# Kernel tuning notes

Hardware: AMD Instinct MI355X
Metric: run time of the kernel (lower is better)

## Reference

```python
import jax, jax.numpy as jnp
import numpy as np

EMBED = 1024
HEADS = 16
HEAD_DIM = EMBED // HEADS
FF = 4 * EMBED
B, S = 2, 2048
EPS = 1e-5


def layer_norm(x, g, b):
    mu = jnp.mean(x, axis=-1, keepdims=True)
    var = jnp.mean(jnp.square(x - mu), axis=-1, keepdims=True)
    return (x - mu) * jax.lax.rsqrt(var + EPS) * g + b


def setup_inputs() -> dict:
    key = jax.random.key(0)
    ks = jax.random.split(key, 12)
    sc = 0.02
    x = jax.random.normal(ks[0], (B, S, EMBED), dtype=jnp.float32)
    # causal mask: 1 where attending allowed (mask==0 -> -inf in original)
    mask = jnp.tril(jnp.ones((S, S), dtype=jnp.int32))[None, None]
    return {
        "x": x,
        "mask": mask,
        "ln1_g": jnp.ones((EMBED,), jnp.float32),
        "ln1_b": jnp.zeros((EMBED,), jnp.float32),
        "wq": sc * jax.random.normal(ks[1], (EMBED, EMBED), jnp.float32),
        "bq": jnp.zeros((EMBED,), jnp.float32),
        "wk": sc * jax.random.normal(ks[2], (EMBED, EMBED), jnp.float32),
        "bk": jnp.zeros((EMBED,), jnp.float32),
        "wv": sc * jax.random.normal(ks[3], (EMBED, EMBED), jnp.float32),
        "bv": jnp.zeros((EMBED,), jnp.float32),
        "wo": sc * jax.random.normal(ks[4], (EMBED, EMBED), jnp.float32),
        "bo": jnp.zeros((EMBED,), jnp.float32),
        "ln2_g": jnp.ones((EMBED,), jnp.float32),
        "ln2_b": jnp.zeros((EMBED,), jnp.float32),
        "w1": sc * jax.random.normal(ks[5], (EMBED, FF), jnp.float32),
        "b1": jnp.zeros((FF,), jnp.float32),
        "w2": sc * jax.random.normal(ks[6], (FF, EMBED), jnp.float32),
        "b2": jnp.zeros((EMBED,), jnp.float32),
    }


def reference(x, mask, ln1_g, ln1_b, wq, bq, wk, bk, wv, bv, wo, bo,
              ln2_g, ln2_b, w1, b1, w2, b2):
    bsz, seq, _ = x.shape
    residual = x
    h = layer_norm(x, ln1_g, ln1_b)
    # QKV projections -> [B, H, S, Dh]
    def split_heads(t):
        return t.reshape(bsz, seq, HEADS, HEAD_DIM).transpose(0, 2, 1, 3)
    q = split_heads(h @ wq + bq)
    k = split_heads(h @ wk + bk)
    v = split_heads(h @ wv + bv)
    scores = jnp.einsum('bhqd,bhkd->bhqk', q, k) / (HEAD_DIM ** 0.5)
    scores = jnp.where(mask == 0, -jnp.inf, scores)
    attn = jax.nn.softmax(scores, axis=-1)
    out = jnp.einsum('bhqk,bhkd->bhqd', attn, v)
    out = out.transpose(0, 2, 1, 3).reshape(bsz, seq, EMBED)
    out = out @ wo + bo
    x = residual + out
    residual = x
    h = layer_norm(x, ln2_g, ln2_b)
    h = jax.nn.gelu(h @ w1 + b1, approximate=False) @ w2 + b2
    return residual + h
```

## Files before the change

### kernel.cpp

```cpp
#include <hip/hip_runtime.h>

typedef unsigned short u16;
typedef unsigned int   u32;
typedef __attribute__((ext_vector_type(8))) short bf16x8;
typedef __attribute__((ext_vector_type(4))) float f32x4;

#define S_LEN 2048
#define EMB   1024
#define NH    16
#define HD    64
#define FF_DIM 4096
#define NROWS 4096

__device__ __forceinline__ float b2f(u16 u){ union{u32 i; float f;} c; c.i = ((u32)u)<<16; return c.f; }
__device__ __forceinline__ u16 f2b(float f){ union{float f; u32 u;} c; c.f=f; return (u16)((c.u + 0x8000u)>>16); }
__device__ __forceinline__ float gelu_f(float x){
    float z  = x * 0.70710678118f;
    float az = fabsf(z);
    float t  = 1.0f / (1.0f + 0.3275911f * az);
    float p  = ((((1.061405429f*t - 1.453152027f)*t + 1.421413741f)*t - 0.284496736f)*t + 0.254829592f)*t;
    float e  = __expf(-az*az);
    float erfv = 1.0f - p*e;
    erfv = (z < 0.f) ? -erfv : erfv;
    return 0.5f*x*(1.0f + erfv);
}

__device__ __forceinline__ void load_lds16(const u16* g, u16* l) {
    __builtin_amdgcn_global_load_lds((const __attribute__((address_space(1))) u32*)g,
                                     (__attribute__((address_space(3))) u32*)l, 16, 0, 0);
}

template<int XF32>
__global__ __launch_bounds__(256)
void ln_kernel(const void* __restrict__ Xv, const float* __restrict__ G,
               const float* __restrict__ Bv, u16* __restrict__ Y)
{
    const int row = blockIdx.x, t = threadIdx.x;
    float v0, v1, v2, v3;
    if constexpr (XF32) {
        float4 r4 = ((const float4*)((const float*)Xv + (size_t)row*EMB))[t];
        v0 = r4.x; v1 = r4.y; v2 = r4.z; v3 = r4.w;
    } else {
        const u16* xr = (const u16*)Xv + (size_t)row*EMB;
        uint2 raw = *(const uint2*)(xr + t*4);
        v0 = b2f(raw.x & 0xffff); v1 = b2f(raw.x >> 16);
        v2 = b2f(raw.y & 0xffff); v3 = b2f(raw.y >> 16);
    }
    float s  = v0+v1+v2+v3;
    float s2 = v0*v0+v1*v1+v2*v2+v3*v3;
    #pragma unroll
    for (int off = 1; off < 64; off <<= 1) {
        s  += __shfl_xor(s,  off, 64);
        s2 += __shfl_xor(s2, off, 64);
    }
    __shared__ float ps[4], ps2[4];
    const int w = t >> 6, lane = t & 63;
    if (lane == 0) { ps[w] = s; ps2[w] = s2; }
    __syncthreads();
    s  = ps[0]+ps[1]+ps[2]+ps[3];
    s2 = ps2[0]+ps2[1]+ps2[2]+ps2[3];
    const float mu   = s * (1.0f/EMB);
    const float rstd = rsqrtf(fmaxf(s2*(1.0f/EMB) - mu*mu, 0.f) + 1e-5f);
    float4 g4 = ((const float4*)G)[t];
    float4 c4 = ((const float4*)Bv)[t];
    u32 lo = (u32)f2b((v0-mu)*rstd*g4.x + c4.x) | ((u32)f2b((v1-mu)*rstd*g4.y + c4.y) << 16);
    u32 hi = (u32)f2b((v2-mu)*rstd*g4.z + c4.z) | ((u32)f2b((v3-mu)*rstd*g4.w + c4.w) << 16);
    uint2 o; o.x = lo; o.y = hi;
    *(uint2*)(Y + (size_t)row*EMB + t*4) = o;
}

__global__ __launch_bounds__(256)
void transpose_k(const float* __restrict__ in, u16* __restrict__ out, int K, int N)
{
    __shared__ __align__(16) u16 T[64*72];
    const int k0 = blockIdx.y*64, n0 = blockIdx.x*64, t = threadIdx.x;
    #pragma unroll
    for (int c = 0; c < 4; ++c) {
        int e = t*4 + c*1024, ki = e >> 6, nj = e & 63;
        float4 f = *(const float4*)(in + (size_t)(k0+ki)*N + n0 + nj);
        ushort4 s4; s4.x = f2b(f.x); s4.y = f2b(f.y); s4.z = f2b(f.z); s4.w = f2b(f.w);
        *(ushort4*)&T[ki*72 + nj] = s4;
    }
    __syncthreads();
    #pragma unroll
    for (int c = 0; c < 2; ++c) {
        int e = t*8 + c*2048, ni = e >> 6, kj = e & 63;
        uint4 v; u16* pv = (u16*)&v;
        #pragma unroll
        for (int j = 0; j < 8; ++j) pv[j] = T[(kj+j)*72 + ni];
        *(uint4*)(out + (size_t)(n0+ni)*K + k0 + kj) = v;
    }
}

__global__ __launch_bounds__(256)
void vtrans(const u16* __restrict__ in, u16* __restrict__ out)
{
    __shared__ __align__(16) u16 T[64*72];
    const int bh = blockIdx.y, s0 = blockIdx.x*64, t = threadIdx.x;
    const size_t base = (size_t)bh * (S_LEN*HD);
    #pragma unroll
    for (int c = 0; c < 2; ++c) {
        int e = t*8 + c*2048, r = e >> 6, d = e & 63;
        *(uint4*)&T[r*72 + d] = *(const uint4*)(in + base + (size_t)(s0 + r)*HD + d);
    }
    __syncthreads();
    #pragma unroll
    for (int c = 0; c < 2; ++c) {
        int e = t*8 + c*2048, d = e >> 6, sj = e & 63;
        uint4 v; u16* pv = (u16*)&v;
        #pragma unroll
        for (int j = 0; j < 8; ++j) pv[j] = T[(sj + j)*72 + d];
        *(uint4*)(out + base + (size_t)d*S_LEN + s0 + sj) = v;
    }
}

__device__ __forceinline__ void stage2(const u16* s0, const u16* s1, int koff, u16* dst, int wave){
    load_lds16(s0 + koff, dst + wave*512);
    load_lds16(s1 + koff, dst + 4096 + wave*512);
}

template<int CBUF, int KS, int NHH, int TAILVM>
__device__ __forceinline__ void phase256(u16* Ls, f32x4 (&acc)[8][4],
    int wm, int wn, int lr, int quad, int wave,
    const u16* s0, const u16* s1, int koff, u16* dst)
{
    const u16* ak = Ls + CBUF*32768 + KS*8192;
    const u16* bk = Ls + CBUF*32768 + 16384 + KS*8192;
    bf16x8 af[8], bf[2];
    #pragma unroll
    for (int mf = 0; mf < 8; ++mf) {
        int off = (wm*128 + mf*16 + lr)*32 + quad*8;
        af[mf] = *(const bf16x8*)(ak + (off ^ ((off>>3)&0x18)));
    }
    #pragma unroll
    for (int nf = 0; nf < 2; ++nf) {
        int off = (wn*64 + NHH*32 + nf*16 + lr)*32 + quad*8;
        bf[nf] = *(const bf16x8*)(bk + (off ^ ((off>>3)&0x18)));
    }
    stage2(s0, s1, koff, dst, wave);
    __builtin_amdgcn_s_barrier();
    __builtin_amdgcn_s_setprio(1);
    #pragma unroll
    for (int mf = 0; mf < 8; ++mf) {
        acc[mf][NHH*2+0] = __builtin_amdgcn_mfma_f32_16x16x32_bf16(af[mf], bf[0], acc[mf][NHH*2+0], 0, 0, 0);
        acc[mf][NHH*2+1] = __builtin_amdgcn_mfma_f32_16x16x32_bf16(af[mf], bf[1], acc[mf][NHH*2+1], 0, 0, 0);
    }
    __builtin_amdgcn_s_setprio(0);
    if constexpr (TAILVM) asm volatile("s_waitcnt vmcnt(8)" ::: "memory");
    __builtin_amdgcn_s_barrier();
}

template<int MODE>
__global__ __launch_bounds__(512, 2)
void gemm256(const u16* __restrict__ A, const u16* __restrict__ Bt,
             const float* __restrict__ bias, const float* __restrict__ bias2,
             const float* __restrict__ bias3,
             void* __restrict__ C, void* __restrict__ C2, void* __restrict__ C3,
             int M, int N, int K)
{
    (void)M;
    __shared__ __align__(16) u16 Ls[65536];
    const int t = threadIdx.x;
    const int wave = t >> 6, lane = t & 63;
    const int wm = wave >> 2, wn = wave & 3;
    const int lr = lane & 15, quad = lane >> 4;
    const int n0 = blockIdx.x*256, m0 = blockIdx.y*256;

    const int c0 = wave*64 + lane, c1 = 512 + wave*64 + lane;
    const int l0 = c0 ^ ((c0 >> 3) & 3), l1 = c1 ^ ((c1 >> 3) & 3);
    const int r0 = l0 >> 2, g0 = l0 & 3;
    const int r1 = l1 >> 2, g1 = l1 & 3;
    const u16* srcA0 = A  + (size_t)(m0 + r0)*K + g0*8;
    const u16* srcA1 = A  + (size_t)(m0 + r1)*K + g1*8;
    const u16* srcB0 = Bt + (size_t)(n0 + r0)*K + g0*8;
    const u16* srcB1 = Bt + (size_t)(n0 + r1)*K + g1*8;

    u16* A00 = Ls + 0;
    u16* A01 = Ls + 8192;
    u16* B00 = Ls + 16384;
    u16* B01 = Ls + 16384 + 8192;
    u16* A10 = Ls + 32768;
    u16* A11 = Ls + 32768 + 8192;
    u16* B10 = Ls + 32768 + 16384;
    u16* B11 = Ls + 32768 + 16384 + 8192;

    f32x4 acc[8][4];
    const f32x4 fzero = {0.f, 0.f, 0.f, 0.f};
    #pragma unroll
    for (int i = 0; i < 8; ++i)
        #pragma unroll
        for (int j = 0; j < 4; ++j) acc[i][j] = fzero;

    const int NT = K >> 6;

    stage2(srcA0, srcA1, 0,   A00, wave);
    stage2(srcB0, srcB1, 0,   B00, wave);
    stage2(srcA0, srcA1, 32,  A01, wave);
    stage2(srcB0, srcB1, 32,  B01, wave);
    stage2(srcA0, srcA1, 64,  A10, wave);
    stage2(srcB0, srcB1, 64,  B10, wave);
    asm volatile("s_waitcnt vmcnt(8)" ::: "memory");
    __builtin_amdgcn_s_barrier();

    for (int U = 0; U < NT; U += 2) {
        const int k1 = ((U+1) & (NT-1))*64;
        const int k2 = ((U+2) & (NT-1))*64;
        const int k3 = ((U+3) & (NT-1))*64;
        phase256<0,0,0,0>(Ls, acc, wm, wn, lr, quad, wave, srcA0, srcA1, k1+32, A11);
        phase256<0,0,1,1>(Ls, acc, wm, wn, lr, quad, wave, srcB0, srcB1, k1+32, B11);
        phase256<0,1,0,0>(Ls, acc, wm, wn, lr, quad, wave, srcA0, srcA1, k2,    A00);
        phase256<0,1,1,1>(Ls, acc, wm, wn, lr, quad, wave, srcB0, srcB1, k2,    B00);
        phase256<1,0,0,0>(Ls, acc, wm, wn, lr, quad, wave, srcA0, srcA1, k2+32, A01);
        phase256<1,0,1,1>(Ls, acc, wm, wn, lr, quad, wave, srcB0, srcB1, k2+32, B01);
        phase256<1,1,0,0>(Ls, acc, wm, wn, lr, quad, wave, srcA0, srcA1, k3,    A10);
        phase256<1,1,1,1>(Ls, acc, wm, wn, lr, quad, wave, srcB0, srcB1, k3,    B10);
    }

    asm volatile("s_waitcnt vmcnt(0)" ::: "memory");
    __syncthreads();

    float bv[4];
    #pragma unroll
    for (int nf = 0; nf < 4; ++nf) {
        const int col = n0 + wn*64 + nf*16 + lr;
        if constexpr (MODE == 5) {
            const int seg = n0 >> 10;
            bv[nf] = (seg == 0 ? bias : (seg == 1 ? bias2 : bias3))[col & 1023];
        } else {
            bv[nf] = bias[col];
        }
    }
    #pragma unroll
    for (int mf = 0; mf < 8; ++mf)
        #pragma unroll
        for (int nf = 0; nf < 4; ++nf)
            #pragma unroll
            for (int r = 0; r < 4; ++r) {
                float v = acc[mf][nf][r] + bv[nf];
                if constexpr (MODE == 2) v = gelu_f(v);
                Ls[(wm*128 + mf*16 + quad*4 + r)*256 + wn*64 + nf*16 + lr] = f2b(v);
            }
    __syncthreads();
    #pragma unroll
    for (int j = 0; j < 16; ++j) {
        const int idx = j*512 + t;
        const int rr = idx >> 5, ck = idx & 31;
        const u16* src = Ls + rr*256 + ck*8;
        const int row = m0 + rr, col = n0 + ck*8;
        if constexpr (MODE == 5) {
            const int seg = n0 >> 10;
            u16* dstb = (u16*)(seg == 0 ? C : (seg == 1 ? C2 : C3));
            const int cs = col & 1023;
            const int h = cs >> 6, d = cs & 63;
            const int b_ = row >> 11, s = row & 2047;
            *(uint4*)(dstb + ((((size_t)(b_*NH + h))*S_LEN + s) << 6) + d) = *(const uint4*)src;
        } else {
            *(uint4*)((u16*)C + (size_t)row*N + col) = *(const uint4*)src;
        }
    }
}

template<int MODE, int RESF, int OUTF, int TM>
__global__ __launch_bounds__(256)
void gemm_bt(const u16* __restrict__ A, const u16* __restrict__ Bt,
             const float* __restrict__ bias, const float* __restrict__ bias2,
             const float* __restrict__ bias3, const void* __restrict__ res,
             void* __restrict__ C, void* __restrict__ C2, void* __restrict__ C3,
             int M, int N, int K)
{
    constexpr int MT  = (TM == 128) ? 4 : 2;
    constexpr int ACH = TM * 32;
    __shared__ __align__(16) u16 Sm[(TM == 128) ? 16384 : 12288];
    u16* As = Sm;
    u16* Bs = Sm + 2*ACH;
    const int t = threadIdx.x;
    const int m0 = (TM == 128) ? blockIdx.y*128 : blockIdx.x*64;
    const int n0 = (TM == 128) ? blockIdx.x*128 : blockIdx.y*128;
    const int wave = t >> 6, lane = t & 63;
    const int wm = (wave >> 1) * (TM/2);
    const int wn = (wave & 1) * 64;
    const int lr = lane & 15, quad = lane >> 4;

    const u16* gA = A  + (size_t)(m0 + wave*16 + (lane >> 2))*K + (lane & 3)*8;
    const u16* gB = Bt + (size_t)(n0 + wave*16 + (lane >> 2))*K + (lane & 3)*8;
    u16* lA = As + wave*512;
    u16* lB = Bs + wave*512;

    f32x4 acc[MT][4];
    const f32x4 fzero = {0.f, 0.f, 0.f, 0.f};
    #pragma unroll
    for (int mt = 0; mt < MT; ++mt)
        #pragma unroll
        for (int nt = 0; nt < 4; ++nt) acc[mt][nt] = fzero;

    for (int kt = 0; kt < K; kt += 64) {
        __syncthreads();
        #pragma unroll
        for (int c = 0; c < 2; ++c) {
            load_lds16(gA + c*32, lA + c*ACH);
            if constexpr (TM == 128)
                load_lds16(gA + (size_t)64*K + c*32, lA + c*ACH + 2048);
            load_lds16(gB + c*32, lB + c*4096);
            load_lds16(gB + (size_t)64*K + c*32, lB + c*4096 + 2048);
        }
        gA += 64; gB += 64;
        __syncthreads();
        #pragma unroll
        for (int ks = 0; ks < 2; ++ks) {
            bf16x8 af[MT], bf[4];
            #pragma unroll
            for (int i = 0; i < MT; ++i)
                af[i] = *(const bf16x8*)&As[ks*ACH + (wm + i*16 + lr)*32 + quad*8];
            #pragma unroll
            for (int i = 0; i < 4; ++i)
                bf[i] = *(const bf16x8*)&Bs[ks*4096 + (wn + i*16 + lr)*32 + quad*8];
            #pragma unroll
            for (int mt = 0; mt < MT; ++mt)
                #pragma unroll
                for (int nt = 0; nt < 4; ++nt)
                    acc[mt][nt] = __builtin_amdgcn_mfma_f32_16x16x32_bf16(af[mt], bf[nt], acc[mt][nt], 0, 0, 0);
        }
    }

    u16* qkvDst = nullptr;
    if constexpr (MODE == 5) {
        int seg = n0 >> 10;
        qkvDst = (u16*)(seg == 0 ? C : (seg == 1 ? C2 : C3));
    }

    #pragma unroll
    for (int c = 0; c < (TM == 128 ? 2 : 1); ++c) {
        __syncthreads();
        if (TM == 64 || (wave >> 1) == c) {
            #pragma unroll
            for (int nt = 0; nt < 4; ++nt) {
                int colL = wn + nt*16 + lr;
                float bval;
                if constexpr (MODE == 5) {
                    int col = n0 + colL;
                    int seg = col >> 10, cs = col & 1023;
                    bval = (seg == 0 ? bias : (seg == 1 ? bias2 : bias3))[cs];
                } else {
                    bval = bias[n0 + colL];
                }
                #pragma unroll
                for (int mt = 0; mt < MT; ++mt) {
                    #pragma unroll
                    for (int r = 0; r < 4; ++r) {
                        int rowL = (TM == 128 ? mt*16 : wm + mt*16) + quad*4 + r;
                        float v = acc[mt][nt][r] + bval;
                        if constexpr (MODE == 2) v = gelu_f(v);
                        Sm[rowL*136 + colL] = f2b(v);
                    }
                }
            }
        }
        __syncthreads();
        #pragma unroll
        for (int i = 0; i < 4; ++i) {
            const int rowL = wave*16 + i*4 + (lane >> 4);
            const int colL = (lane & 15)*8;
            const int row  = m0 + c*64 + rowL;
            const u16* src = &Sm[rowL*136 + colL];
            if constexpr (MODE == 5) {
                int cs = (n0 + colL) & 1023;
                int h = cs >> 6, d = cs & 63;
                int b_ = row >> 11, s = row & 2047;
                u16* dst = qkvDst + ((((size_t)(b_*NH + h))*S_LEN + s) << 6) + d;
                *(uint4*)dst = *(const uint4*)src;
            } else {
                size_t base = (size_t)row*N + n0 + colL;
                if constexpr (MODE == 1 || OUTF) {
                    uint4 sv = *(const uint4*)src;
                    const u16* sp = (const u16*)&sv;
                    float f[8];
                    #pragma unroll
                    for (int j = 0; j < 8; ++j) f[j] = b2f(sp[j]);
                    if constexpr (MODE == 1) {
                        if constexpr (RESF) {
                            const float* rp = (const float*)res + base;
                            float4 r0 = *(const float4*)rp, r1 = *(const float4*)(rp+4);
                            f[0]+=r0.x; f[1]+=r0.y; f[2]+=r0.z; f[3]+=r0.w;
                            f[4]+=r1.x; f[5]+=r1.y; f[6]+=r1.z; f[7]+=r1.w;
                        } else {
                            uint4 rv = *(const uint4*)((const u16*)res + base);
                            const u16* rp = (const u16*)&rv;
                            #pragma unroll
                            for (int j = 0; j < 8; ++j) f[j] += b2f(rp[j]);
                        }
                    }
                    if constexpr (OUTF) {
                        float* op = (float*)C + base;
                        float4 o0 = {f[0],f[1],f[2],f[3]}, o1 = {f[4],f[5],f[6],f[7]};
                        *(float4*)op = o0; *(float4*)(op+4) = o1;
                    } else {
                        u16 ov[8];
                        #pragma unroll
                        for (int j = 0; j < 8; ++j) ov[j] = f2b(f[j]);
                        *(uint4*)((u16*)C + base) = *(const uint4*)ov;
                    }
                } else {
                    *(uint4*)((u16*)C + base) = *(const uint4*)src;
                }
            }
        }
    }
}

__global__ __launch_bounds__(256, 2)
void attn_kernel(const u16* __restrict__ Q, const u16* __restrict__ Kg,
                 const u16* __restrict__ Vt, u16* __restrict__ O)
{
    const int bh = blockIdx.x;
    const int pr = blockIdx.y;
    const int qta = pr, qtb = 31 - pr;
    const int t = threadIdx.x, wave = t >> 6, lane = t & 63;
    const int lr = lane & 15, quad = lane >> 4;

    __shared__ __align__(16) u16 Ks[4096];
    __shared__ __align__(16) u16 Vs[4096];
    __shared__ __align__(16) u16 Ps[4][16*72];

    const size_t qkbase = (size_t)bh * (S_LEN*HD);
    const int b = bh >> 4, h = bh & 15;
    u16* Pw = Ps[wave];
    const f32x4 fzero = {0.f, 0.f, 0.f, 0.f};

    const u16* qpa = Q + qkbase + (size_t)(qta*64 + wave*16 + lr)*HD + quad*8;
    const u16* qpb = Q + qkbase + (size_t)(qtb*64 + wave*16 + lr)*HD + quad*8;
    bf16x8 qa0 = *(const bf16x8*)qpa, qa1 = *(const bf16x8*)(qpa + 32);
    bf16x8 qb0 = *(const bf16x8*)qpb, qb1 = *(const bf16x8*)(qpb + 32);

    f32x4 oa[4], ob[4];
    float la[4], lb[4];
    #pragma unroll
    for (int dt = 0; dt < 4; ++dt) { oa[dt] = fzero; ob[dt] = fzero; }
    #pragma unroll
    for (int r = 0; r < 4; ++r) { la[r] = 0.f; lb[r] = 0.f; }

    const u16* gK = Kg + qkbase + (size_t)(wave*16 + (lane>>2))*HD + (lane&3)*8;
    const u16* gV = Vt + qkbase + (size_t)(wave*16 + (lane>>2))*S_LEN + (lane&3)*8;
    u16* lK = Ks + wave*512;
    u16* lV = Vs + wave*512;

    const int qrow_qa = qta*64 + wave*16 + quad*4;
    const int qrow_qb = qtb*64 + wave*16 + quad*4;

    for (int kb = 0; kb <= qtb; ++kb) {
        __syncthreads();
        load_lds16(gK + (size_t)kb*4096,      lK);
        load_lds16(gK + (size_t)kb*4096 + 32, lK + 2048);
        load_lds16(gV + kb*64,                lV);
        load_lds16(gV + kb*64 + 32,           lV + 2048);
        __syncthreads();

        #pragma unroll
        for (int tile = 0; tile < 2; ++tile) {
            const int qt = tile ? qta : qtb;
            if (tile && kb > qta) break;
            bf16x8 qf0 = tile ? qa0 : qb0;
            bf16x8 qf1 = tile ? qa1 : qb1;
            f32x4* oacc = tile ? oa : ob;
            float* lp   = tile ? la : lb;
            const int qrowq = tile ? qrow_qa : qrow_qb;

            f32x4 sc[4];
            #pragma unroll
            for (int kt2 = 0; kt2 < 4; ++kt2) {
                bf16x8 kf0 = *(const bf16x8*)&Ks[(kt2*16 + lr)*32 + quad*8];
                bf16x8 kf1 = *(const bf16x8*)&Ks[2048 + (kt2*16 + lr)*32 + quad*8];
                sc[kt2] = __builtin_amdgcn_mfma_f32_16x16x32_bf16(qf0, kf0, fzero, 0, 0, 0);
                sc[kt2] = __builtin_amdgcn_mfma_f32_16x16x32_bf16(qf1, kf1, sc[kt2], 0, 0, 0);
            }
            const bool diag = (kb == qt);
            #pragma unroll
            for (int r = 0; r < 4; ++r) {
                #pragma unroll
                for (int kt2 = 0; kt2 < 4; ++kt2) {
                    int kcol = kb*64 + kt2*16 + lr;
                    float p = (!diag || kcol <= qrowq + r) ? __expf(fminf(sc[kt2][r]*0.125f, 30.f)) : 0.f;
                    lp[r] += p;
                    Pw[(quad*4 + r)*72 + kt2*16 + lr] = f2b(p);
                }
            }
            bf16x8 pf0 = *(const bf16x8*)&Pw[lr*72 + quad*8];
            bf16x8 pf1 = *(const bf16x8*)&Pw[lr*72 + 32 + quad*8];
            #pragma unroll
            for (int dt = 0; dt < 4; ++dt) {
                bf16x8 vf0 = *(const bf16x8*)&Vs[(dt*16 + lr)*32 + quad*8];
                bf16x8 vf1 = *(const bf16x8*)&Vs[2048 + (dt*16 + lr)*32 + quad*8];
                oacc[dt] = __builtin_amdgcn_mfma_f32_16x16x32_bf16(pf0, vf0, oacc[dt], 0, 0, 0);
                oacc[dt] = __builtin_amdgcn_mfma_f32_16x16x32_bf16(pf1, vf1, oacc[dt], 0, 0, 0);
            }
        }
    }

    #pragma unroll
    for (int tile = 0; tile < 2; ++tile) {
        const int qt = tile ? qta : qtb;
        f32x4* oacc = tile ? oa : ob;
        float* lp   = tile ? la : lb;
        #pragma unroll
        for (int r = 0; r < 4; ++r) {
            float v = lp[r];
            v += __shfl_xor(v, 1, 64); v += __shfl_xor(v, 2, 64);
            v += __shfl_xor(v, 4, 64); v += __shfl_xor(v, 8, 64);
            lp[r] = 1.0f / fmaxf(v, 1e-20f);
        }
        #pragma unroll
        for (int dt = 0; dt < 4; ++dt)
            #pragma unroll
            for (int r = 0; r < 4; ++r)
                Pw[(quad*4 + r)*64 + dt*16 + lr] = f2b(oacc[dt][r] * lp[r]);

        const int q = lane >> 2, d0 = (lane & 3)*16;
        u16* dst = O + ((size_t)(b*S_LEN + qt*64 + wave*16 + q))*EMB + h*HD + d0;
        *(uint4*)(dst)     = *(uint4*)&Pw[q*64 + d0];
        *(uint4*)(dst + 8) = *(uint4*)&Pw[q*64 + d0 + 8];
    }
}

extern "C" void kernel_launch(void* const* d_in, const int* in_sizes, int n_in,
                              void* d_out, int out_size, void* d_ws, size_t ws_size,
                              hipStream_t stream)
{
    (void)in_sizes; (void)n_in; (void)out_size; (void)ws_size;
    const float* x    = (const float*)d_in[0];
    const float* ln1g = (const float*)d_in[2];
    const float* ln1b = (const float*)d_in[3];
    const float* wq = (const float*)d_in[4];  const float* bq = (const float*)d_in[5];
    const float* wk = (const float*)d_in[6];  const float* bk = (const float*)d_in[7];
    const float* wv = (const float*)d_in[8];  const float* bv = (const float*)d_in[9];
    const float* wo = (const float*)d_in[10]; const float* bo = (const float*)d_in[11];
    const float* ln2g = (const float*)d_in[12]; const float* ln2b = (const float*)d_in[13];
    const float* w1 = (const float*)d_in[14]; const float* b1 = (const float*)d_in[15];
    const float* w2 = (const float*)d_in[16]; const float* b2 = (const float*)d_in[17];

    u16* ws = (u16*)d_ws;
    const size_t M1 = 1u << 20;
    u16* wqkvT = ws + 0*M1;
    u16* wqT = ws + 0*M1;
    u16* wkT = ws + 1*M1;
    u16* wvT = ws + 2*M1;
    u16* woT = ws + 3*M1;
    u16* w2T = ws + 0*M1;
    u16* w1T = ws + 4*M1;
    u16* h0  = ws + 8*M1;
    u16* qb  = ws + 12*M1;
    u16* kb  = ws + 16*M1;
    u16* vT  = ws + 20*M1;
    u16* ao  = ws + 24*M1;
    u16* vb  = ws + 24*M1;
    u16* x1  = ws + 28*M1;
    u16* fb  = ws + 12*M1;

    dim3 blk(256);
    transpose_k<<<dim3(16,16), blk, 0, stream>>>(wq, wqT, EMB, EMB);
    transpose_k<<<dim3(16,16), blk, 0, stream>>>(wk, wkT, EMB, EMB);
    transpose_k<<<dim3(16,16), blk, 0, stream>>>(wv, wvT, EMB, EMB);
    transpose_k<<<dim3(16,16), blk, 0, stream>>>(wo, woT, EMB, EMB);
    transpose_k<<<dim3(64,16), blk, 0, stream>>>(w1, w1T, EMB, FF_DIM);

    ln_kernel<1><<<NROWS, blk, 0, stream>>>(x, ln1g, ln1b, h0);

    gemm256<5><<<dim3(12,16), dim3(512), 0, stream>>>(h0, wqkvT, bq, bk, bv,
                                                      qb, kb, vb, NROWS, 3072, EMB);

    vtrans<<<dim3(32,32), blk, 0, stream>>>(vb, vT);

    attn_kernel<<<dim3(32,16), blk, 0, stream>>>(qb, kb, vT, ao);

    gemm_bt<1,1,0,64><<<dim3(64,8), blk, 0, stream>>>(ao, woT, bo, nullptr, nullptr, x,
                                                      x1, nullptr, nullptr, NROWS, EMB, EMB);

    transpose_k<<<dim3(16,64), blk, 0, stream>>>(w2, w2T, FF_DIM, EMB);

    ln_kernel<0><<<NROWS, blk, 0, stream>>>(x1, ln2g, ln2b, h0);

    gemm256<2><<<dim3(16,16), dim3(512), 0, stream>>>(h0, w1T, b1, nullptr, nullptr,
                                                      fb, nullptr, nullptr, NROWS, FF_DIM, EMB);

    gemm_bt<1,0,1,64><<<dim3(64,8), blk, 0, stream>>>(fb, w2T, b2, nullptr, nullptr, x1,
                                                      d_out, nullptr, nullptr, NROWS, EMB, FF_DIM);
}
```

Baseline: 374.6 us.

## Use split-K 256x256 pipelined GEMM with reduction kernels for Wo and FF2

Replaces the simple 64x128-tile GEMM used for the output projection and the second feed-forward layer with the pipelined 256x256-tile GEMM core. K is split four ways to give 256 blocks. Each split writes bf16 partial sums, and separate elementwise kernels add the partials, bias and residual. The main loop is factored into a shared device function. This adds extra global traffic for the partials and extra launches. Storing partials in bf16 reduces accuracy, and the output buffer is reused as scratch space.

```diff
diff --git a/kernel.cpp b/kernel.cpp
--- a/kernel.cpp
+++ b/kernel.cpp
@@ -150,31 +150,10 @@
     __builtin_amdgcn_s_barrier();
 }
 
-template<int MODE>
-__global__ __launch_bounds__(512, 2)
-void gemm256(const u16* __restrict__ A, const u16* __restrict__ Bt,
-             const float* __restrict__ bias, const float* __restrict__ bias2,
-             const float* __restrict__ bias3,
-             void* __restrict__ C, void* __restrict__ C2, void* __restrict__ C3,
-             int M, int N, int K)
-{
-    (void)M;
-    __shared__ __align__(16) u16 Ls[65536];
-    const int t = threadIdx.x;
-    const int wave = t >> 6, lane = t & 63;
-    const int wm = wave >> 2, wn = wave & 3;
-    const int lr = lane & 15, quad = lane >> 4;
-    const int n0 = blockIdx.x*256, m0 = blockIdx.y*256;
-
-    const int c0 = wave*64 + lane, c1 = 512 + wave*64 + lane;
-    const int l0 = c0 ^ ((c0 >> 3) & 3), l1 = c1 ^ ((c1 >> 3) & 3);
-    const int r0 = l0 >> 2, g0 = l0 & 3;
-    const int r1 = l1 >> 2, g1 = l1 & 3;
-    const u16* srcA0 = A  + (size_t)(m0 + r0)*K + g0*8;
-    const u16* srcA1 = A  + (size_t)(m0 + r1)*K + g1*8;
-    const u16* srcB0 = Bt + (size_t)(n0 + r0)*K + g0*8;
-    const u16* srcB1 = Bt + (size_t)(n0 + r1)*K + g1*8;
-
+__device__ __forceinline__ void gemm256_main(u16* Ls, f32x4 (&acc)[8][4],
+    int wm, int wn, int lr, int quad, int wave, int NT,
+    const u16* srcA0, const u16* srcA1, const u16* srcB0, const u16* srcB1)
+{
     u16* A00 = Ls + 0;
     u16* A01 = Ls + 8192;
     u16* B00 = Ls + 16384;
@@ -183,15 +162,6 @@
     u16* A11 = Ls + 32768 + 8192;
     u16* B10 = Ls + 32768 + 16384;
     u16* B11 = Ls + 32768 + 16384 + 8192;
-
-    f32x4 acc[8][4];
-    const f32x4 fzero = {0.f, 0.f, 0.f, 0.f};
-    #pragma unroll
-    for (int i = 0; i < 8; ++i)
-        #pragma unroll
-        for (int j = 0; j < 4; ++j) acc[i][j] = fzero;
-
-    const int NT = K >> 6;
 
     stage2(srcA0, srcA1, 0,   A00, wave);
     stage2(srcB0, srcB1, 0,   B00, wave);
@@ -218,6 +188,41 @@
 
     asm volatile("s_waitcnt vmcnt(0)" ::: "memory");
     __syncthreads();
+}
+
+template<int MODE>
+__global__ __launch_bounds__(512, 2)
+void gemm256(const u16* __restrict__ A, const u16* __restrict__ Bt,
+             const float* __restrict__ bias, const float* __restrict__ bias2,
+             const float* __restrict__ bias3,
+             void* __restrict__ C, void* __restrict__ C2, void* __restrict__ C3,
+             int M, int N, int K)
+{
+    (void)M;
+    __shared__ __align__(16) u16 Ls[65536];
+    const int t = threadIdx.x;
+    const int wave = t >> 6, lane = t & 63;
+    const int wm = wave >> 2, wn = wave & 3;
+    const int lr = lane & 15, quad = lane >> 4;
+    const int n0 = blockIdx.x*256, m0 = blockIdx.y*256;
+
+    const int c0 = wave*64 + lane, c1 = 512 + wave*64 + lane;
+    const int l0 = c0 ^ ((c0 >> 3) & 3), l1 = c1 ^ ((c1 >> 3) & 3);
+    const int r0 = l0 >> 2, g0 = l0 & 3;
+    const int r1 = l1 >> 2, g1 = l1 & 3;
+    const u16* srcA0 = A  + (size_t)(m0 + r0)*K + g0*8;
+    const u16* srcA1 = A  + (size_t)(m0 + r1)*K + g1*8;
+    const u16* srcB0 = Bt + (size_t)(n0 + r0)*K + g0*8;
+    const u16* srcB1 = Bt + (size_t)(n0 + r1)*K + g1*8;
+
+    f32x4 acc[8][4];
+    const f32x4 fzero = {0.f, 0.f, 0.f, 0.f};
+    #pragma unroll
+    for (int i = 0; i < 8; ++i)
+        #pragma unroll
+        for (int j = 0; j < 4; ++j) acc[i][j] = fzero;
+
+    gemm256_main(Ls, acc, wm, wn, lr, quad, wave, K >> 6, srcA0, srcA1, srcB0, srcB1);
 
     float bv[4];
     #pragma unroll
@@ -260,151 +265,113 @@
     }
 }
 
-template<int MODE, int RESF, int OUTF, int TM>
+__global__ __launch_bounds__(512, 2)
+void gemm256sk(const u16* __restrict__ A, const u16* __restrict__ Bt,
+               u16* __restrict__ Cl, u16* __restrict__ Ch, int N, int K)
+{
+    __shared__ __align__(16) u16 Ls[65536];
+    const int t = threadIdx.x;
+    const int wave = t >> 6, lane = t & 63;
+    const int wm = wave >> 2, wn = wave & 3;
+    const int lr = lane & 15, quad = lane >> 4;
+    const int n0 = blockIdx.x*256, m0 = blockIdx.y*256;
+    const int z  = blockIdx.z;
+    const int Ks = K >> 2;
+
+    const int c0 = wave*64 + lane, c1 = 512 + wave*64 + lane;
+    const int l0 = c0 ^ ((c0 >> 3) & 3), l1 = c1 ^ ((c1 >> 3) & 3);
+    const int r0 = l0 >> 2, g0 = l0 & 3;
+    const int r1 = l1 >> 2, g1 = l1 & 3;
+    const u16* srcA0 = A  + (size_t)(m0 + r0)*K + g0*8 + z*Ks;
+    const u16* srcA1 = A  + (size_t)(m0 + r1)*K + g1*8 + z*Ks;
+    const u16* srcB0 = Bt + (size_t)(n0 + r0)*K + g0*8 + z*Ks;
+    const u16* srcB1 = Bt + (size_t)(n0 + r1)*K + g1*8 + z*Ks;
+
+    f32x4 acc[8][4];
+    const f32x4 fzero = {0.f, 0.f, 0.f, 0.f};
+    #pragma unroll
+    for (int i = 0; i < 8; ++i)
+        #pragma unroll
+        for (int j = 0; j < 4; ++j) acc[i][j] = fzero;
+
+    gemm256_main(Ls, acc, wm, wn, lr, quad, wave, Ks >> 6, srcA0, srcA1, srcB0, srcB1);
+
+    #pragma unroll
+    for (int mf = 0; mf < 8; ++mf)
+        #pragma unroll
+        for (int nf = 0; nf < 4; ++nf)
+            #pragma unroll
+            for (int r = 0; r < 4; ++r)
+                Ls[(wm*128 + mf*16 + quad*4 + r)*256 + wn*64 + nf*16 + lr] = f2b(acc[mf][nf][r]);
+    __syncthreads();
+    u16* dst = (z < 2 ? Cl : Ch) + (size_t)(z & 1)*(1u<<22);
+    #pragma unroll
+    for (int j = 0; j < 16; ++j) {
+        const int idx = j*512 + t;
+        const int rr = idx >> 5, ck = idx & 31;
+        *(uint4*)(dst + (size_t)(m0 + rr)*N + n0 + ck*8) = *(const uint4*)(Ls + rr*256 + ck*8);
+    }
+}
+
 __global__ __launch_bounds__(256)
-void gemm_bt(const u16* __restrict__ A, const u16* __restrict__ Bt,
-             const float* __restrict__ bias, const float* __restrict__ bias2,
-             const float* __restrict__ bias3, const void* __restrict__ res,
-             void* __restrict__ C, void* __restrict__ C2, void* __restrict__ C3,
-             int M, int N, int K)
-{
-    constexpr int MT  = (TM == 128) ? 4 : 2;
-    constexpr int ACH = TM * 32;
-    __shared__ __align__(16) u16 Sm[(TM == 128) ? 16384 : 12288];
-    u16* As = Sm;
-    u16* Bs = Sm + 2*ACH;
-    const int t = threadIdx.x;
-    const int m0 = (TM == 128) ? blockIdx.y*128 : blockIdx.x*64;
-    const int n0 = (TM == 128) ? blockIdx.x*128 : blockIdx.y*128;
-    const int wave = t >> 6, lane = t & 63;
-    const int wm = (wave >> 1) * (TM/2);
-    const int wn = (wave & 1) * 64;
-    const int lr = lane & 15, quad = lane >> 4;
-
-    const u16* gA = A  + (size_t)(m0 + wave*16 + (lane >> 2))*K + (lane & 3)*8;
-    const u16* gB = Bt + (size_t)(n0 + wave*16 + (lane >> 2))*K + (lane & 3)*8;
-    u16* lA = As + wave*512;
-    u16* lB = Bs + wave*512;
-
-    f32x4 acc[MT][4];
-    const f32x4 fzero = {0.f, 0.f, 0.f, 0.f};
-    #pragma unroll
-    for (int mt = 0; mt < MT; ++mt)
-        #pragma unroll
-        for (int nt = 0; nt < 4; ++nt) acc[mt][nt] = fzero;
-
-    for (int kt = 0; kt < K; kt += 64) {
-        __syncthreads();
-        #pragma unroll
-        for (int c = 0; c < 2; ++c) {
-            load_lds16(gA + c*32, lA + c*ACH);
-            if constexpr (TM == 128)
-                load_lds16(gA + (size_t)64*K + c*32, lA + c*ACH + 2048);
-            load_lds16(gB + c*32, lB + c*4096);
-            load_lds16(gB + (size_t)64*K + c*32, lB + c*4096 + 2048);
-        }
-        gA += 64; gB += 64;
-        __syncthreads();
-        #pragma unroll
-        for (int ks = 0; ks < 2; ++ks) {
-            bf16x8 af[MT], bf[4];
-            #pragma unroll
-            for (int i = 0; i < MT; ++i)
-                af[i] = *(const bf16x8*)&As[ks*ACH + (wm + i*16 + lr)*32 + quad*8];
-            #pragma unroll
-            for (int i = 0; i < 4; ++i)
-                bf[i] = *(const bf16x8*)&Bs[ks*4096 + (wn + i*16 + lr)*32 + quad*8];
-            #pragma unroll
-            for (int mt = 0; mt < MT; ++mt)
-                #pragma unroll
-                for (int nt = 0; nt < 4; ++nt)
-                    acc[mt][nt] = __builtin_amdgcn_mfma_f32_16x16x32_bf16(af[mt], bf[nt], acc[mt][nt], 0, 0, 0);
-        }
-    }
-
-    u16* qkvDst = nullptr;
-    if constexpr (MODE == 5) {
-        int seg = n0 >> 10;
-        qkvDst = (u16*)(seg == 0 ? C : (seg == 1 ? C2 : C3));
-    }
-
-    #pragma unroll
-    for (int c = 0; c < (TM == 128 ? 2 : 1); ++c) {
-        __syncthreads();
-        if (TM == 64 || (wave >> 1) == c) {
-            #pragma unroll
-            for (int nt = 0; nt < 4; ++nt) {
-                int colL = wn + nt*16 + lr;
-                float bval;
-                if constexpr (MODE == 5) {
-                    int col = n0 + colL;
-                    int seg = col >> 10, cs = col & 1023;
-                    bval = (seg == 0 ? bias : (seg == 1 ? bias2 : bias3))[cs];
-                } else {
-                    bval = bias[n0 + colL];
-                }
-                #pragma unroll
-                for (int mt = 0; mt < MT; ++mt) {
-                    #pragma unroll
-                    for (int r = 0; r < 4; ++r) {
-                        int rowL = (TM == 128 ? mt*16 : wm + mt*16) + quad*4 + r;
-                        float v = acc[mt][nt][r] + bval;
-                        if constexpr (MODE == 2) v = gelu_f(v);
-                        Sm[rowL*136 + colL] = f2b(v);
-                    }
-                }
-            }
-        }
-        __syncthreads();
-        #pragma unroll
-        for (int i = 0; i < 4; ++i) {
-            const int rowL = wave*16 + i*4 + (lane >> 4);
-            const int colL = (lane & 15)*8;
-            const int row  = m0 + c*64 + rowL;
-            const u16* src = &Sm[rowL*136 + colL];
-            if constexpr (MODE == 5) {
-                int cs = (n0 + colL) & 1023;
-                int h = cs >> 6, d = cs & 63;
-                int b_ = row >> 11, s = row & 2047;
-                u16* dst = qkvDst + ((((size_t)(b_*NH + h))*S_LEN + s) << 6) + d;
-                *(uint4*)dst = *(const uint4*)src;
-            } else {
-                size_t base = (size_t)row*N + n0 + colL;
-                if constexpr (MODE == 1 || OUTF) {
-                    uint4 sv = *(const uint4*)src;
-                    const u16* sp = (const u16*)&sv;
-                    float f[8];
-                    #pragma unroll
-                    for (int j = 0; j < 8; ++j) f[j] = b2f(sp[j]);
-                    if constexpr (MODE == 1) {
-                        if constexpr (RESF) {
-                            const float* rp = (const float*)res + base;
-                            float4 r0 = *(const float4*)rp, r1 = *(const float4*)(rp+4);
-                            f[0]+=r0.x; f[1]+=r0.y; f[2]+=r0.z; f[3]+=r0.w;
-                            f[4]+=r1.x; f[5]+=r1.y; f[6]+=r1.z; f[7]+=r1.w;
-                        } else {
-                            uint4 rv = *(const uint4*)((const u16*)res + base);
-                            const u16* rp = (const u16*)&rv;
-                            #pragma unroll
-                            for (int j = 0; j < 8; ++j) f[j] += b2f(rp[j]);
-                        }
-                    }
-                    if constexpr (OUTF) {
-                        float* op = (float*)C + base;
-                        float4 o0 = {f[0],f[1],f[2],f[3]}, o1 = {f[4],f[5],f[6],f[7]};
-                        *(float4*)op = o0; *(float4*)(op+4) = o1;
-                    } else {
-                        u16 ov[8];
-                        #pragma unroll
-                        for (int j = 0; j < 8; ++j) ov[j] = f2b(f[j]);
-                        *(uint4*)((u16*)C + base) = *(const uint4*)ov;
-                    }
-                } else {
-                    *(uint4*)((u16*)C + base) = *(const uint4*)src;
-                }
-            }
-        }
-    }
+void reduce_wo(const u16* __restrict__ pl, const u16* __restrict__ ph,
+               const float* __restrict__ xres, const float* __restrict__ bias,
+               u16* __restrict__ y)
+{
+    const int i0 = (blockIdx.x*256 + threadIdx.x)*8;
+    uint4 a0 = *(const uint4*)(pl + i0);
+    uint4 a1 = *(const uint4*)(pl + (1u<<22) + i0);
+    uint4 a2 = *(const uint4*)(ph + i0);
+    uint4 a3 = *(const uint4*)(ph + (1u<<22) + i0);
+    const int col = i0 & 1023;
+    float4 b0 = *(const float4*)(bias + col);
+    float4 b1 = *(const float4*)(bias + col + 4);
+    float4 x0 = *(const float4*)(xres + i0);
+    float4 x1 = *(const float4*)(xres + i0 + 4);
+    const u16 *s0=(const u16*)&a0, *s1=(const u16*)&a1, *s2=(const u16*)&a2, *s3=(const u16*)&a3;
+    const float bb[8] = {b0.x,b0.y,b0.z,b0.w,b1.x,b1.y,b1.z,b1.w};
+    const float xx[8] = {x0.x,x0.y,x0.z,x0.w,x1.x,x1.y,x1.z,x1.w};
+    u16 out[8];
+    #pragma unroll
+    for (int j = 0; j < 8; ++j)
+        out[j] = f2b(b2f(s0[j]) + b2f(s1[j]) + b2f(s2[j]) + b2f(s3[j]) + bb[j] + xx[j]);
+    *(uint4*)(y + i0) = *(const uint4*)out;
+}
+
+__global__ __launch_bounds__(256)
+void reduce_sum4(u16* __restrict__ pl, const u16* __restrict__ ph)
+{
+    const int i0 = (blockIdx.x*256 + threadIdx.x)*8;
+    uint4 a0 = *(const uint4*)(pl + i0);
+    uint4 a1 = *(const uint4*)(pl + (1u<<22) + i0);
+    uint4 a2 = *(const uint4*)(ph + i0);
+    uint4 a3 = *(const uint4*)(ph + (1u<<22) + i0);
+    const u16 *s0=(const u16*)&a0, *s1=(const u16*)&a1, *s2=(const u16*)&a2, *s3=(const u16*)&a3;
+    u16 out[8];
+    #pragma unroll
+    for (int j = 0; j < 8; ++j)
+        out[j] = f2b(b2f(s0[j]) + b2f(s1[j]) + b2f(s2[j]) + b2f(s3[j]));
+    *(uint4*)(pl + i0) = *(const uint4*)out;
+}
+
+__global__ __launch_bounds__(256)
+void final_ff2(const u16* __restrict__ s, const u16* __restrict__ x1b,
+               const float* __restrict__ bias, float* __restrict__ out)
+{
+    const int i0 = (blockIdx.x*256 + threadIdx.x)*8;
+    uint4 a = *(const uint4*)(s + i0);
+    uint4 xr = *(const uint4*)(x1b + i0);
+    const int col = i0 & 1023;
+    float4 b0 = *(const float4*)(bias + col);
+    float4 b1 = *(const float4*)(bias + col + 4);
+    const u16 *sp=(const u16*)&a, *xp=(const u16*)&xr;
+    const float bb[8] = {b0.x,b0.y,b0.z,b0.w,b1.x,b1.y,b1.z,b1.w};
+    float f[8];
+    #pragma unroll
+    for (int j = 0; j < 8; ++j) f[j] = b2f(sp[j]) + b2f(xp[j]) + bb[j];
+    float4 o0 = {f[0],f[1],f[2],f[3]}, o1 = {f[4],f[5],f[6],f[7]};
+    *(float4*)(out + i0) = o0;
+    *(float4*)(out + i0 + 4) = o1;
 }
 
 __global__ __launch_bounds__(256, 2)
@@ -553,6 +520,8 @@
     u16* vb  = ws + 24*M1;
     u16* x1  = ws + 28*M1;
     u16* fb  = ws + 12*M1;
+    u16* wosl = ws + 8*M1;
+    u16* ffsl = ws + 4*M1;
 
     dim3 blk(256);
     transpose_k<<<dim3(16,16), blk, 0, stream>>>(wq, wqT, EMB, EMB);
@@ -570,8 +539,8 @@
 
     attn_kernel<<<dim3(32,16), blk, 0, stream>>>(qb, kb, vT, ao);
 
-    gemm_bt<1,1,0,64><<<dim3(64,8), blk, 0, stream>>>(ao, woT, bo, nullptr, nullptr, x,
-                                                      x1, nullptr, nullptr, NROWS, EMB, EMB);
+    gemm256sk<<<dim3(4,16,4), dim3(512), 0, stream>>>(ao, woT, wosl, wosl + 8*M1, EMB, EMB);
+    reduce_wo<<<2048, blk, 0, stream>>>(wosl, wosl + 8*M1, x, bo, x1);
 
     transpose_k<<<dim3(16,64), blk, 0, stream>>>(w2, w2T, FF_DIM, EMB);
 
@@ -580,6 +549,7 @@
     gemm256<2><<<dim3(16,16), dim3(512), 0, stream>>>(h0, w1T, b1, nullptr, nullptr,
                                                       fb, nullptr, nullptr, NROWS, FF_DIM, EMB);
 
-    gemm_bt<1,0,1,64><<<dim3(64,8), blk, 0, stream>>>(fb, w2T, b2, nullptr, nullptr, x1,
-                                                      d_out, nullptr, nullptr, NROWS, EMB, FF_DIM);
-}
+    gemm256sk<<<dim3(4,16,4), dim3(512), 0, stream>>>(fb, w2T, ffsl, (u16*)d_out, EMB, FF_DIM);
+    reduce_sum4<<<2048, blk, 0, stream>>>(ffsl, (u16*)d_out);
+    final_ff2<<<2048, blk, 0, stream>>>(ffsl, x1, b2, (float*)d_out);
+}
```

Result: no change. 373.3 us (-0.3%).
